# Kernel tuning notes

Hardware: AMD Instinct MI355X
Metric: run time of the kernel (lower is better)

Reference implementation:

```python
import jax, jax.numpy as jnp
import numpy as np

DIM = 768
NUM_HEADS = 12
H_SCALE = 1000.0


def setup_inputs() -> dict:
    key = jax.random.key(0)
    ks = jax.random.split(key, 6)
    B, N, C = 4, 1024, DIM
    x = jax.random.normal(ks[0], (B, N, C), dtype=jnp.float32)
    # elevations in meters: uniform in [0, 3000)
    elevation_patches = jax.random.uniform(ks[1], (B, N), dtype=jnp.float32) * 3000.0
    # torch nn.Linear weights are [out_features, in_features]
    W_qkv = jax.random.normal(ks[2], (3 * C, C), dtype=jnp.float32) * (1.0 / np.sqrt(C))
    W_proj = jax.random.normal(ks[3], (C, C), dtype=jnp.float32) * (1.0 / np.sqrt(C))
    b_proj = jnp.zeros((C,), dtype=jnp.float32)
    alpha = jnp.asarray(1.0, dtype=jnp.float32)
    return {"x": x, "elevation_patches": elevation_patches, "W_qkv": W_qkv,
            "W_proj": W_proj, "b_proj": b_proj, "alpha": alpha}


def reference(x, elevation_patches, W_qkv, W_proj, b_proj, alpha):
    B, N, C = x.shape
    H = NUM_HEADS
    hd = C // H
    scale = hd ** -0.5
    # qkv projection (no bias): [B, N, 3C] -> [3, B, H, N, hd]
    qkv = (x @ W_qkv.T).reshape(B, N, 3, H, hd).transpose(2, 0, 3, 1, 4)
    q, k, v = qkv[0], qkv[1], qkv[2]
    # scores: [B, H, N, N]
    scores = jnp.einsum("bhid,bhjd->bhij", q, k) * scale
    # elevation bias: penalty for uphill attention (j higher than i)
    elev_diff = (elevation_patches[:, None, :] - elevation_patches[:, :, None]) / H_SCALE
    bias = jnp.clip(-alpha * jax.nn.relu(elev_diff), -10.0, 0.0)  # [B, N, N]
    scores = scores + bias[:, None, :, :]
    attn = jax.nn.softmax(scores, axis=-1)
    # output: [B, H, N, hd] -> [B, N, C]
    out = jnp.einsum("bhij,bhjd->bhid", attn, v).transpose(0, 2, 1, 3).reshape(B, N, C)
    return out @ W_proj.T + b_proj
```

## Files before the change

kernel.cpp:

```cpp
#include <hip/hip_runtime.h>
#include <stdint.h>

typedef _Float16 f16;
typedef __attribute__((ext_vector_type(8))) _Float16 half8;
typedef __attribute__((ext_vector_type(4))) _Float16 half4;
typedef __attribute__((ext_vector_type(4))) float f32x4;

#define BATCH   4
#define NSEQ    1024
#define DIMC    768
#define NHEADS  12
#define HDIM    64
#define CQKV    2304
#define MROWS   4096
#define LOG2E   1.4426950408889634f
#define SCLQ    (0.125f * LOG2E)
#define CLIP2   (10.0f * LOG2E)

__device__ __forceinline__ void gload_lds16(const void* g, void* l) {
    __builtin_amdgcn_global_load_lds(
        (const __attribute__((address_space(1))) void*)g,
        (__attribute__((address_space(3))) void*)l, 16, 0, 0);
}

__global__ void cvt3_kernel(const float* __restrict__ x, const float* __restrict__ wq,
                            const float* __restrict__ wp,
                            f16* __restrict__ xf, f16* __restrict__ wqf,
                            f16* __restrict__ wpf) {
    const int A0 = MROWS * DIMC / 4;
    const int A1 = A0 + CQKV * DIMC / 4;
    const int A2 = A1 + DIMC * DIMC / 4;
    int i = blockIdx.x * blockDim.x + threadIdx.x;
    if (i >= A2) return;
    const float* src; f16* dst; int j;
    if (i < A0)      { src = x;  dst = xf;  j = i; }
    else if (i < A1) { src = wq; dst = wqf; j = i - A0; }
    else             { src = wp; dst = wpf; j = i - A1; }
    float4 v = reinterpret_cast<const float4*>(src)[j];
    half4 h;
    h.x = (f16)v.x; h.y = (f16)v.y; h.z = (f16)v.z; h.w = (f16)v.w;
    reinterpret_cast<half4*>(dst)[j] = h;
}

template <int EPI, int BM, int BN>
__global__ __launch_bounds__(256, 3)
void gemm_f16(const f16* __restrict__ A, const f16* __restrict__ B, int Kdim,
              f16* __restrict__ qf, f16* __restrict__ kf, f16* __restrict__ vtf,
              float* __restrict__ outp, const float* __restrict__ bias) {
    constexpr int MF = BM / 32, NF = BN / 32;
    constexpr int CA = BM * 4, CB = BN * 4;
    constexpr int LPT = (BM + BN) / 64;
    __shared__ __align__(16) f16 lA[2][BM * 32];
    __shared__ __align__(16) f16 lB[2][BN * 32];
    const int tid = threadIdx.x;
    const int w = tid >> 6, lane = tid & 63;
    const int l15 = lane & 15, lg = lane >> 4;
    const int m0 = blockIdx.y * BM, n0 = blockIdx.x * BN;
    const int wm = w >> 1, wn = w & 1;

    auto stage = [&](int k0, int buf) {
#pragma unroll
        for (int r = 0; r < CA / 256; ++r) {
            int chunk = r * 256 + tid;
            int row = chunk >> 2, c8 = chunk & 3;
            int s = c8 ^ ((row >> 1) & 3);
            gload_lds16(A + (size_t)(m0 + row) * Kdim + k0 + s * 8,
                        &lA[buf][chunk * 8]);
        }
#pragma unroll
        for (int r = 0; r < CB / 256; ++r) {
            int chunk = r * 256 + tid;
            int row = chunk >> 2, c8 = chunk & 3;
            int s = c8 ^ ((row >> 1) & 3);
            gload_lds16(B + (size_t)(n0 + row) * Kdim + k0 + s * 8,
                        &lB[buf][chunk * 8]);
        }
    };

    f32x4 acc[MF][NF] = {};

    stage(0, 0);

    const int slotA = lg ^ ((l15 >> 1) & 3);
    const int nst = Kdim / 32;
    int cur = 0;
    for (int t = 0; t < nst; ++t) {
        if (t + 1 < nst) {
            stage((t + 1) * 32, cur ^ 1);
            if constexpr (LPT == 4)
                asm volatile("s_waitcnt vmcnt(4)" ::: "memory");
            else
                asm volatile("s_waitcnt vmcnt(2)" ::: "memory");
        } else {
            asm volatile("s_waitcnt vmcnt(0)" ::: "memory");
        }
        __builtin_amdgcn_s_barrier();
        __builtin_amdgcn_sched_barrier(0);

        half8 af[MF], bf[NF];
#pragma unroll
        for (int i = 0; i < MF; ++i) {
            int row = wm * (BM / 2) + i * 16 + l15;
            af[i] = *(const half8*)&lA[cur][row * 32 + slotA * 8];
        }
#pragma unroll
        for (int j = 0; j < NF; ++j) {
            int row = wn * (BN / 2) + j * 16 + l15;
            bf[j] = *(const half8*)&lB[cur][row * 32 + slotA * 8];
        }
#pragma unroll
        for (int m = 0; m < MF; ++m)
#pragma unroll
            for (int n = 0; n < NF; ++n)
                acc[m][n] = __builtin_amdgcn_mfma_f32_16x16x32_f16(af[m], bf[n], acc[m][n], 0, 0, 0);

        __builtin_amdgcn_sched_barrier(0);
        __builtin_amdgcn_s_barrier();
        cur ^= 1;
    }

    if constexpr (EPI == 0) {
#pragma unroll
        for (int n = 0; n < NF; ++n) {
            int col = n0 + wn * (BN / 2) + n * 16 + l15;
            int sec = col / 768;
            int rem = col - sec * 768;
            int hh = rem >> 6, dd = rem & 63;
#pragma unroll
            for (int m = 0; m < MF; ++m) {
                int rb = m0 + wm * (BM / 2) + m * 16 + 4 * lg;
                int b = rb >> 10, i0 = rb & 1023;
                if (sec == 0) {
#pragma unroll
                    for (int r = 0; r < 4; ++r)
                        qf[((size_t)(b * NHEADS + hh) * NSEQ + i0 + r) * HDIM + dd] =
                            (f16)(acc[m][n][r] * SCLQ);
                } else if (sec == 1) {
#pragma unroll
                    for (int r = 0; r < 4; ++r)
                        kf[((size_t)(b * NHEADS + hh) * NSEQ + i0 + r) * HDIM + dd] =
                            (f16)acc[m][n][r];
                } else {
                    half4 hv;
                    hv.x = (f16)acc[m][n][0]; hv.y = (f16)acc[m][n][1];
                    hv.z = (f16)acc[m][n][2]; hv.w = (f16)acc[m][n][3];
                    *(half4*)&vtf[((size_t)(b * NHEADS + hh) * HDIM + dd) * NSEQ + i0] = hv;
                }
            }
        }
    } else {
#pragma unroll
        for (int n = 0; n < NF; ++n) {
            int col = n0 + wn * (BN / 2) + n * 16 + l15;
            float bv = bias[col];
#pragma unroll
            for (int m = 0; m < MF; ++m) {
                int rb = m0 + wm * (BM / 2) + m * 16 + 4 * lg;
#pragma unroll
                for (int r = 0; r < 4; ++r)
                    outp[(size_t)(rb + r) * DIMC + col] = acc[m][n][r] + bv;
            }
        }
    }
}

__global__ __launch_bounds__(256, 3)
void attn_f16(const f16* __restrict__ qf, const f16* __restrict__ kf,
              const f16* __restrict__ vtf, const float* __restrict__ elev,
              const float* __restrict__ alphap, f16* __restrict__ aof) {
    __shared__ __align__(16) f16 lK[2][64 * 64];
    __shared__ __align__(16) f16 lV[2][64 * 64];
    __shared__ __align__(16) f16 lP[4][1024];
    __shared__ __align__(16) float lElev[NSEQ];
    const int tid = threadIdx.x;
    const int w = tid >> 6, lane = tid & 63;
    const int l15 = lane & 15, lg = lane >> 4;

    const int bid = blockIdx.x;
    const int lid = (bid & 7) * 96 + (bid >> 3);
    const int q0 = (lid & 15) * 64;
    const int bh = lid >> 4;
    const int b = bh / NHEADS, h = bh - b * NHEADS;
    const float esc = alphap[0] * (LOG2E * 0.001f);
    const size_t base = (size_t)bh * NSEQ * HDIM;
    const size_t vbase = (size_t)bh * HDIM * NSEQ;

    const int ch0 = tid, ch1 = 256 + tid;
    const int r0 = ch0 >> 3, s0 = ((ch0 & 7) ^ (r0 & 7)) * 8;
    const int r1 = ch1 >> 3, s1 = ((ch1 & 7) ^ (r1 & 7)) * 8;

    auto stageKV = [&](int j0, int buf) {
        gload_lds16(kf + base + (size_t)(j0 + r0) * HDIM + s0, &lK[buf][ch0 * 8]);
        gload_lds16(kf + base + (size_t)(j0 + r1) * HDIM + s1, &lK[buf][ch1 * 8]);
        gload_lds16(vtf + vbase + (size_t)r0 * NSEQ + j0 + s0, &lV[buf][ch0 * 8]);
        gload_lds16(vtf + vbase + (size_t)r1 * NSEQ + j0 + s1, &lV[buf][ch1 * 8]);
    };

    stageKV(0, 0);

    {
        float4 e4 = reinterpret_cast<const float4*>(elev + b * NSEQ)[tid];
        *reinterpret_cast<float4*>(&lElev[tid * 4]) = e4;
    }
    half8 qa[2];
    {
        int qrow = q0 + w * 16 + l15;
#pragma unroll
        for (int ks = 0; ks < 2; ++ks)
            qa[ks] = *(const half8*)&qf[base + (size_t)qrow * HDIM + ks * 32 + 8 * lg];
    }
    __syncthreads();

    float ei2[4];
#pragma unroll
    for (int r = 0; r < 4; ++r)
        ei2[r] = lElev[q0 + w * 16 + 4 * lg + r] * esc;

    float prs[4] = {0.f, 0.f, 0.f, 0.f};
    f32x4 o[4] = {};

    const int sswz = l15 & 7;
    int cur = 0;
    for (int j0 = 0; j0 < NSEQ; j0 += 64) {
        if (j0 + 64 < NSEQ) stageKV(j0 + 64, cur ^ 1);

        f32x4 s[4] = {};
        __builtin_amdgcn_s_setprio(1);
#pragma unroll
        for (int n = 0; n < 4; ++n)
#pragma unroll
            for (int ks = 0; ks < 2; ++ks) {
                int slot = (ks * 4 + lg) ^ sswz;
                half8 kb8 = *(const half8*)&lK[cur][(n * 16 + l15) * 64 + slot * 8];
                s[n] = __builtin_amdgcn_mfma_f32_16x16x32_f16(qa[ks], kb8, s[n], 0, 0, 0);
            }
        __builtin_amdgcn_s_setprio(0);

#pragma unroll
        for (int n = 0; n < 4; ++n) {
            float ej = lElev[j0 + n * 16 + l15];
#pragma unroll
            for (int r = 0; r < 4; ++r) {
                float d2 = fmaf(ej, esc, -ei2[r]);
                float p = __builtin_amdgcn_exp2f(
                    s[n][r] - fminf(fmaxf(d2, 0.f), CLIP2));
                prs[r] += p;
                int prow = 4 * lg + r;
                int idx = prow * 64 + ((2 * n + (l15 >> 3)) ^ (prow & 7)) * 8 + (l15 & 7);
                lP[w][idx] = (f16)p;
            }
        }

        __builtin_amdgcn_s_setprio(1);
#pragma unroll
        for (int ks = 0; ks < 2; ++ks) {
            half8 pa = *(const half8*)&lP[w][l15 * 64 + ((ks * 4 + lg) ^ sswz) * 8];
#pragma unroll
            for (int df = 0; df < 4; ++df) {
                int slot = (ks * 4 + lg) ^ sswz;
                half8 vb = *(const half8*)&lV[cur][(df * 16 + l15) * 64 + slot * 8];
                o[df] = __builtin_amdgcn_mfma_f32_16x16x32_f16(pa, vb, o[df], 0, 0, 0);
            }
        }
        __builtin_amdgcn_s_setprio(0);

        asm volatile("s_waitcnt vmcnt(0)" ::: "memory");
        __builtin_amdgcn_s_barrier();
        cur ^= 1;
    }

#pragma unroll
    for (int r = 0; r < 4; ++r) {
        prs[r] += __shfl_xor(prs[r], 1);
        prs[r] += __shfl_xor(prs[r], 2);
        prs[r] += __shfl_xor(prs[r], 4);
        prs[r] += __shfl_xor(prs[r], 8);
    }

#pragma unroll
    for (int r = 0; r < 4; ++r) {
        float inv = 1.0f / prs[r];
        int row = q0 + w * 16 + 4 * lg + r;
        size_t ob = ((size_t)b * NSEQ + row) * DIMC + h * HDIM;
#pragma unroll
        for (int df = 0; df < 4; ++df)
            aof[ob + df * 16 + l15] = (f16)(o[df][r] * inv);
    }
}

extern "C" void kernel_launch(void* const* d_in, const int* in_sizes, int n_in,
                              void* d_out, int out_size, void* d_ws, size_t ws_size,
                              hipStream_t stream) {
    const float* x     = (const float*)d_in[0];
    const float* elev  = (const float*)d_in[1];
    const float* wqkv  = (const float*)d_in[2];
    const float* wproj = (const float*)d_in[3];
    const float* bproj = (const float*)d_in[4];
    const float* alpha = (const float*)d_in[5];
    float* out = (float*)d_out;

    char* ws = (char*)d_ws;
    size_t off = 0;
    auto alloc = [&](size_t elems) {
        void* p = ws + off;
        off += (elems * 2 + 255) & ~(size_t)255;
        return (f16*)p;
    };
    const size_t szXW  = (size_t)MROWS * DIMC;
    const size_t szWQ  = (size_t)CQKV * DIMC;
    const size_t szWP  = (size_t)DIMC * DIMC;
    const size_t szQKV = (size_t)BATCH * NHEADS * NSEQ * HDIM;

    f16* xf  = alloc(szXW);
    f16* wqf = alloc(szWQ);
    f16* wpf = alloc(szWP);
    f16* qf  = alloc(szQKV);
    f16* kf  = alloc(szQKV);
    f16* vtf = alloc(szQKV);
    f16* aof = xf;
    (void)ws_size; (void)in_sizes; (void)n_in; (void)out_size;

    const int n4 = (int)((szXW + szWQ + szWP) / 4);
    cvt3_kernel<<<(n4 + 255) / 256, 256, 0, stream>>>(x, wqkv, wproj, xf, wqf, wpf);

    gemm_f16<0, 128, 128><<<dim3(CQKV / 128, MROWS / 128), 256, 0, stream>>>(
        xf, wqf, DIMC, qf, kf, vtf, nullptr, nullptr);

    attn_f16<<<BATCH * NHEADS * (NSEQ / 64), 256, 0, stream>>>(
        qf, kf, vtf, elev, alpha, aof);

    gemm_f16<1, 64, 64><<<dim3(DIMC / 64, MROWS / 64), 256, 0, stream>>>(
        aof, wpf, DIMC, nullptr, nullptr, nullptr, out, bproj);
}
```

Before: 84.87 us.

## Double KV tile width to 128 and read V directly from global memory

The attention loop now processes 128 keys per iteration instead of 64, staging only K into LDS with double buffering. V fragments are loaded straight from global memory inside the PV MFMA loop instead of going through LDS. The P scratch buffer is widened and its swizzle changed to match. This halves the barrier count and frees LDS, but V loads now sit on the critical path of the MFMAs with exposed global latency, and register pressure rises with 8 score accumulators.

```diff
diff --git a/kernel.cpp b/kernel.cpp
--- a/kernel.cpp
+++ b/kernel.cpp
@@ -168,9 +168,8 @@
 void attn_f16(const f16* __restrict__ qf, const f16* __restrict__ kf,
               const f16* __restrict__ vtf, const float* __restrict__ elev,
               const float* __restrict__ alphap, f16* __restrict__ aof) {
-    __shared__ __align__(16) f16 lK[2][64 * 64];
-    __shared__ __align__(16) f16 lV[2][64 * 64];
-    __shared__ __align__(16) f16 lP[4][1024];
+    __shared__ __align__(16) f16 lK[2][128 * 64];
+    __shared__ __align__(16) f16 lP[4][2048];
     __shared__ __align__(16) float lElev[NSEQ];
     const int tid = threadIdx.x;
     const int w = tid >> 6, lane = tid & 63;
@@ -185,18 +184,17 @@
     const size_t base = (size_t)bh * NSEQ * HDIM;
     const size_t vbase = (size_t)bh * HDIM * NSEQ;
 
-    const int ch0 = tid, ch1 = 256 + tid;
-    const int r0 = ch0 >> 3, s0 = ((ch0 & 7) ^ (r0 & 7)) * 8;
-    const int r1 = ch1 >> 3, s1 = ((ch1 & 7) ^ (r1 & 7)) * 8;
-
-    auto stageKV = [&](int j0, int buf) {
-        gload_lds16(kf + base + (size_t)(j0 + r0) * HDIM + s0, &lK[buf][ch0 * 8]);
-        gload_lds16(kf + base + (size_t)(j0 + r1) * HDIM + s1, &lK[buf][ch1 * 8]);
-        gload_lds16(vtf + vbase + (size_t)r0 * NSEQ + j0 + s0, &lV[buf][ch0 * 8]);
-        gload_lds16(vtf + vbase + (size_t)r1 * NSEQ + j0 + s1, &lV[buf][ch1 * 8]);
+    auto stageK = [&](int j0, int buf) {
+#pragma unroll
+        for (int r = 0; r < 4; ++r) {
+            int c = r * 256 + tid;
+            int row = c >> 3;
+            int s = ((c & 7) ^ (row & 7)) * 8;
+            gload_lds16(kf + base + (size_t)(j0 + row) * HDIM + s, &lK[buf][c * 8]);
+        }
     };
 
-    stageKV(0, 0);
+    stageK(0, 0);
 
     {
         float4 e4 = reinterpret_cast<const float4*>(elev + b * NSEQ)[tid];
@@ -221,13 +219,15 @@
 
     const int sswz = l15 & 7;
     int cur = 0;
-    for (int j0 = 0; j0 < NSEQ; j0 += 64) {
-        if (j0 + 64 < NSEQ) stageKV(j0 + 64, cur ^ 1);
-
-        f32x4 s[4] = {};
+    for (int j0 = 0; j0 < NSEQ; j0 += 128) {
+        if (j0 + 128 < NSEQ) stageK(j0 + 128, cur ^ 1);
+
+        f32x4 s[8];
+#pragma unroll
+        for (int n = 0; n < 8; ++n) s[n] = (f32x4){0.f, 0.f, 0.f, 0.f};
         __builtin_amdgcn_s_setprio(1);
 #pragma unroll
-        for (int n = 0; n < 4; ++n)
+        for (int n = 0; n < 8; ++n)
 #pragma unroll
             for (int ks = 0; ks < 2; ++ks) {
                 int slot = (ks * 4 + lg) ^ sswz;
@@ -237,7 +237,7 @@
         __builtin_amdgcn_s_setprio(0);
 
 #pragma unroll
-        for (int n = 0; n < 4; ++n) {
+        for (int n = 0; n < 8; ++n) {
             float ej = lElev[j0 + n * 16 + l15];
 #pragma unroll
             for (int r = 0; r < 4; ++r) {
@@ -246,19 +246,21 @@
                     s[n][r] - fminf(fmaxf(d2, 0.f), CLIP2));
                 prs[r] += p;
                 int prow = 4 * lg + r;
-                int idx = prow * 64 + ((2 * n + (l15 >> 3)) ^ (prow & 7)) * 8 + (l15 & 7);
-                lP[w][idx] = (f16)p;
+                int grp = (2 * n + (l15 >> 3)) ^ prow;
+                lP[w][prow * 128 + grp * 8 + (l15 & 7)] = (f16)p;
             }
         }
 
         __builtin_amdgcn_s_setprio(1);
 #pragma unroll
-        for (int ks = 0; ks < 2; ++ks) {
-            half8 pa = *(const half8*)&lP[w][l15 * 64 + ((ks * 4 + lg) ^ sswz) * 8];
+        for (int ks = 0; ks < 4; ++ks) {
+            int pgrp = (ks * 4 + lg) ^ l15;
+            half8 pa = *(const half8*)&lP[w][l15 * 128 + pgrp * 8];
 #pragma unroll
             for (int df = 0; df < 4; ++df) {
-                int slot = (ks * 4 + lg) ^ sswz;
-                half8 vb = *(const half8*)&lV[cur][(df * 16 + l15) * 64 + slot * 8];
+                const f16* vp = vtf + vbase + (size_t)(df * 16 + l15) * NSEQ
+                                + j0 + ks * 32 + 8 * lg;
+                half8 vb = *(const half8*)vp;
                 o[df] = __builtin_amdgcn_mfma_f32_16x16x32_f16(pa, vb, o[df], 0, 0, 0);
             }
         }
```

Measured after the change: 111.1 us. 31.0% more time.

## Keep attention probabilities in registers via transposed MFMA and lane shuffles

Applied to the files above, without the earlier changes.

Swaps the MFMA operand order so each lane holds scores for one query row across four key columns. The probabilities are then packed into half2 registers and redistributed with cross-lane shuffles to form the A operand of the PV MFMA, which removes the per-warp LDS staging buffer for P. This cuts LDS traffic and LDS footprint, and the occupancy hint is raised from 3 to 4 blocks per CU. The row-sum reduction becomes two shuffles and output stores are vectorized as half4. The cost is eight shuffles per k-step plus selects, and possible register pressure under the tighter launch bound.

```diff
diff --git a/kernel.cpp b/kernel.cpp
--- a/kernel.cpp
+++ b/kernel.cpp
@@ -4,7 +4,9 @@
 typedef _Float16 f16;
 typedef __attribute__((ext_vector_type(8))) _Float16 half8;
 typedef __attribute__((ext_vector_type(4))) _Float16 half4;
+typedef __attribute__((ext_vector_type(2))) _Float16 half2v;
 typedef __attribute__((ext_vector_type(4))) float f32x4;
+typedef __attribute__((ext_vector_type(4))) int int4v;
 
 #define BATCH   4
 #define NSEQ    1024
@@ -21,6 +23,12 @@
     __builtin_amdgcn_global_load_lds(
         (const __attribute__((address_space(1))) void*)g,
         (__attribute__((address_space(3))) void*)l, 16, 0, 0);
+}
+
+__device__ __forceinline__ int packh2(float a, float b) {
+    half2v h;
+    h.x = (f16)a; h.y = (f16)b;
+    return __builtin_bit_cast(int, h);
 }
 
 __global__ void cvt3_kernel(const float* __restrict__ x, const float* __restrict__ wq,
@@ -164,13 +172,12 @@
     }
 }
 
-__global__ __launch_bounds__(256, 3)
+__global__ __launch_bounds__(256, 4)
 void attn_f16(const f16* __restrict__ qf, const f16* __restrict__ kf,
               const f16* __restrict__ vtf, const float* __restrict__ elev,
               const float* __restrict__ alphap, f16* __restrict__ aof) {
     __shared__ __align__(16) f16 lK[2][64 * 64];
     __shared__ __align__(16) f16 lV[2][64 * 64];
-    __shared__ __align__(16) f16 lP[4][1024];
     __shared__ __align__(16) float lElev[NSEQ];
     const int tid = threadIdx.x;
     const int w = tid >> 6, lane = tid & 63;
@@ -211,12 +218,9 @@
     }
     __syncthreads();
 
-    float ei2[4];
-#pragma unroll
-    for (int r = 0; r < 4; ++r)
-        ei2[r] = lElev[q0 + w * 16 + 4 * lg + r] * esc;
-
-    float prs[4] = {0.f, 0.f, 0.f, 0.f};
+    const float ei2 = lElev[q0 + w * 16 + l15] * esc;
+
+    float prs = 0.f;
     f32x4 o[4] = {};
 
     const int sswz = l15 & 7;
@@ -232,34 +236,45 @@
             for (int ks = 0; ks < 2; ++ks) {
                 int slot = (ks * 4 + lg) ^ sswz;
                 half8 kb8 = *(const half8*)&lK[cur][(n * 16 + l15) * 64 + slot * 8];
-                s[n] = __builtin_amdgcn_mfma_f32_16x16x32_f16(qa[ks], kb8, s[n], 0, 0, 0);
+                s[n] = __builtin_amdgcn_mfma_f32_16x16x32_f16(kb8, qa[ks], s[n], 0, 0, 0);
             }
         __builtin_amdgcn_s_setprio(0);
 
+        int pk[4][2];
 #pragma unroll
         for (int n = 0; n < 4; ++n) {
-            float ej = lElev[j0 + n * 16 + l15];
+            float4 e4 = *(const float4*)&lElev[j0 + n * 16 + 4 * lg];
+            float ejr[4] = {e4.x, e4.y, e4.z, e4.w};
+            float p[4];
 #pragma unroll
             for (int r = 0; r < 4; ++r) {
-                float d2 = fmaf(ej, esc, -ei2[r]);
-                float p = __builtin_amdgcn_exp2f(
+                float d2 = fmaf(ejr[r], esc, -ei2);
+                p[r] = __builtin_amdgcn_exp2f(
                     s[n][r] - fminf(fmaxf(d2, 0.f), CLIP2));
-                prs[r] += p;
-                int prow = 4 * lg + r;
-                int idx = prow * 64 + ((2 * n + (l15 >> 3)) ^ (prow & 7)) * 8 + (l15 & 7);
-                lP[w][idx] = (f16)p;
-            }
+                prs += p[r];
+            }
+            pk[n][0] = packh2(p[0], p[1]);
+            pk[n][1] = packh2(p[2], p[3]);
         }
 
         __builtin_amdgcn_s_setprio(1);
 #pragma unroll
         for (int ks = 0; ks < 2; ++ks) {
-            half8 pa = *(const half8*)&lP[w][l15 * 64 + ((ks * 4 + lg) ^ sswz) * 8];
+            int vals[4];
+#pragma unroll
+            for (int u = 0; u < 4; ++u) {
+                int src = l15 + 16 * (2 * (lg & 1) + (u >> 1));
+                int vlo = __shfl(pk[2 * ks][u & 1], src);
+                int vhi = __shfl(pk[2 * ks + 1][u & 1], src);
+                vals[u] = (lg & 2) ? vhi : vlo;
+            }
+            int4v vi = {vals[0], vals[1], vals[2], vals[3]};
+            half8 pa = __builtin_bit_cast(half8, vi);
 #pragma unroll
             for (int df = 0; df < 4; ++df) {
                 int slot = (ks * 4 + lg) ^ sswz;
                 half8 vb = *(const half8*)&lV[cur][(df * 16 + l15) * 64 + slot * 8];
-                o[df] = __builtin_amdgcn_mfma_f32_16x16x32_f16(pa, vb, o[df], 0, 0, 0);
+                o[df] = __builtin_amdgcn_mfma_f32_16x16x32_f16(vb, pa, o[df], 0, 0, 0);
             }
         }
         __builtin_amdgcn_s_setprio(0);
@@ -269,22 +284,22 @@
         cur ^= 1;
     }
 
-#pragma unroll
-    for (int r = 0; r < 4; ++r) {
-        prs[r] += __shfl_xor(prs[r], 1);
-        prs[r] += __shfl_xor(prs[r], 2);
-        prs[r] += __shfl_xor(prs[r], 4);
-        prs[r] += __shfl_xor(prs[r], 8);
-    }
-
-#pragma unroll
-    for (int r = 0; r < 4; ++r) {
-        float inv = 1.0f / prs[r];
-        int row = q0 + w * 16 + 4 * lg + r;
+    prs += __shfl_xor(prs, 16);
+    prs += __shfl_xor(prs, 32);
+
+    {
+        float inv = 1.0f / prs;
+        int row = q0 + w * 16 + l15;
         size_t ob = ((size_t)b * NSEQ + row) * DIMC + h * HDIM;
 #pragma unroll
-        for (int df = 0; df < 4; ++df)
-            aof[ob + df * 16 + l15] = (f16)(o[df][r] * inv);
+        for (int df = 0; df < 4; ++df) {
+            half4 hv;
+            hv.x = (f16)(o[df][0] * inv);
+            hv.y = (f16)(o[df][1] * inv);
+            hv.z = (f16)(o[df][2] * inv);
+            hv.w = (f16)(o[df][3] * inv);
+            *(half4*)&aof[ob + df * 16 + 4 * lg] = hv;
+        }
     }
 }
 
```

Result: slower. 86.88 us (+2.4%).
